# Performance work log

Hardware: AMD Instinct MI355X
Metric: run time of the kernel (lower is better)

Reference implementation:

```python
import jax, jax.numpy as jnp
import numpy as np

N = 100000
E = 1600000
F_IN, F_HID, F_OUT = 128, 32, 2


def setup_inputs() -> dict:
    key = jax.random.key(0)
    k1, k2, k3, k4 = jax.random.split(key, 4)
    x = jax.random.normal(k1, (N, F_IN), dtype=jnp.float32)
    edge_index = jax.random.randint(k2, (2, E), 0, N, dtype=jnp.int64)
    # Glorot-style init like torch_geometric GCNConv
    W1 = jax.random.normal(k3, (F_IN, F_HID), dtype=jnp.float32) * (1.0 / np.sqrt(F_IN))
    b1 = jnp.zeros((F_HID,), dtype=jnp.float32)
    W2 = jax.random.normal(k4, (F_HID, F_OUT), dtype=jnp.float32) * (1.0 / np.sqrt(F_HID))
    b2 = jnp.zeros((F_OUT,), dtype=jnp.float32)
    return {"x": x, "edge_index": edge_index, "W1": W1, "b1": b1, "W2": W2, "b2": b2}


def _gcn_conv(x, row, col, norm, W, b):
    # GCNConv: transform, then normalized aggregate (source -> target), then bias
    h = x @ W                                   # [N, F_out]
    msg = norm[:, None] * h[row]                # gather + scale, [E+N, F_out]
    out = jax.ops.segment_sum(msg, col, num_segments=N)  # scatter-add to targets
    return out + b


def reference(x, edge_index, W1, b1, W2, b2):
    # add self-loops (GCNConv default)
    loops = jnp.arange(N, dtype=edge_index.dtype)
    row = jnp.concatenate([edge_index[0], loops])
    col = jnp.concatenate([edge_index[1], loops])
    # symmetric normalization: deg^{-1/2}[row] * deg^{-1/2}[col], deg = in-degree w/ self-loops
    deg = jax.ops.segment_sum(jnp.ones_like(col, dtype=x.dtype), col, num_segments=N)
    dinv = jnp.where(deg > 0, jax.lax.rsqrt(deg), 0.0)
    norm = dinv[row] * dinv[col]                # [E+N]

    h = _gcn_conv(x, row, col, norm, W1, b1)
    h = jax.nn.relu(h)
    h = _gcn_conv(h, row, col, norm, W2, b2)
    return jax.nn.log_softmax(h, axis=1)
```

## Files before the change

kernel.cpp:

```cpp
#include <hip/hip_runtime.h>
#include <hip/hip_bf16.h>
#include <math.h>
#include <stdint.h>


#define GNN_N 100000
#define GNN_E 1600000
#define NBUCK 391
#define CAP 4608
#define CH 3125

typedef float fx2 __attribute__((ext_vector_type(2)));

__global__ __launch_bounds__(256) void k_bucket(const int* __restrict__ row,
                                                const int* __restrict__ col,
                                                int* __restrict__ bucket_fill,
                                                uint32_t* __restrict__ slab) {
    __shared__ int hist[NBUCK];
    __shared__ int base[NBUCK];
    const int tid = threadIdx.x;
    const int e0 = blockIdx.x * CH;

    int cc[13], rr[13];
    #pragma unroll
    for (int t = 0; t < 12; ++t) {
        cc[t] = col[e0 + tid + t * 256];
        rr[t] = row[e0 + tid + t * 256];
    }
    const bool has12 = (tid < CH - 12 * 256);
    if (has12) { cc[12] = col[e0 + tid + 3072]; rr[12] = row[e0 + tid + 3072]; }

    for (int i = tid; i < NBUCK; i += 256) hist[i] = 0;
    __syncthreads();
    #pragma unroll
    for (int t = 0; t < 12; ++t) atomicAdd(&hist[cc[t] >> 8], 1);
    if (has12) atomicAdd(&hist[cc[12] >> 8], 1);
    __syncthreads();
    for (int i = tid; i < NBUCK; i += 256) {
        int bb = (i + blockIdx.x * 131) % NBUCK;
        base[bb] = atomicAdd(&bucket_fill[bb], hist[bb]);
    }
    __syncthreads();
    #pragma unroll
    for (int t = 0; t < 12; ++t) {
        int b = cc[t] >> 8;
        int p = atomicAdd(&base[b], 1);
        if (p < CAP)
            slab[(size_t)b * CAP + p] = ((uint32_t)rr[t] << 8) | (uint32_t)(cc[t] & 255);
    }
    if (has12) {
        int b = cc[12] >> 8;
        int p = atomicAdd(&base[b], 1);
        if (p < CAP)
            slab[(size_t)b * CAP + p] = ((uint32_t)rr[12] << 8) | (uint32_t)(cc[12] & 255);
    }
}

__global__ __launch_bounds__(512) void k_fine(const uint32_t* __restrict__ slab,
                                              const int* __restrict__ bucket_fill,
                                              int* __restrict__ sorted_row,
                                              int* __restrict__ cnt,
                                              int* __restrict__ offsets,
                                              float* __restrict__ dinv, int n) {
    __shared__ int hist[256];
    __shared__ int excl[256];
    __shared__ int cur[256];
    __shared__ int wsum[4];
    __shared__ int s_gbase;
    __shared__ uint32_t stage[CAP];
    const int tid = threadIdx.x;
    const int b0 = blockIdx.x * 2;
    const int lane = tid & 63, wave = tid >> 6;

    if (tid < 64) {
        int s = 0;
        for (int i = tid; i < b0; i += 64) s += bucket_fill[i];
        #pragma unroll
        for (int m = 32; m >= 1; m >>= 1) s += __shfl_xor(s, m);
        if (tid == 0) s_gbase = s;
    }
    __syncthreads();
    int gbase = s_gbase;

    for (int pass = 0; pass < 2; ++pass) {
        const int b = b0 + pass;
        if (b >= NBUCK) break;
        const int nb = min(bucket_fill[b], CAP);
        const uint32_t* sl = slab + (size_t)b * CAP;

        if (tid < 256) { hist[tid] = 0; cur[tid] = 0; }
        __syncthreads();
        for (int i = tid; i < nb; i += 512)
            atomicAdd(&hist[sl[i] & 255u], 1);
        __syncthreads();
        int v = 0, inc = 0;
        if (tid < 256) {
            v = hist[tid];
            inc = v;
            #pragma unroll
            for (int d = 1; d < 64; d <<= 1) {
                int t = __shfl_up(inc, d);
                if (lane >= d) inc += t;
            }
            if (lane == 63) wsum[wave] = inc;
        }
        __syncthreads();
        if (tid == 0) {
            int a = 0;
            #pragma unroll
            for (int w = 0; w < 4; ++w) { int t = wsum[w]; wsum[w] = a; a += t; }
        }
        __syncthreads();
        if (tid < 256) {
            int ex = inc - v + wsum[wave];
            excl[tid] = ex;
            int c = b * 256 + tid;
            if (c < n) {
                cnt[c] = v;
                offsets[c] = gbase + ex;
                dinv[c] = rsqrtf((float)(v + 1));
            }
        }
        __syncthreads();
        for (int i = tid; i < nb; i += 512) {
            uint32_t u = sl[i];
            int f = (int)(u & 255u);
            int p = atomicAdd(&cur[f], 1);
            stage[excl[f] + p] = u >> 8;
        }
        __syncthreads();
        for (int i = tid; i < nb; i += 512)
            sorted_row[gbase + i] = (int)stage[i];
        gbase += nb;
        __syncthreads();
    }
}

#define MM1_NODES 64
__global__ __launch_bounds__(256) void k_matmul1(const float* __restrict__ x,
                                                 const float* __restrict__ W1,
                                                 const float* __restrict__ dinv,
                                                 uint32_t* __restrict__ h1q, int n) {
    __shared__ float xs[MM1_NODES * 129];
    __shared__ float w1s[128 * 32];
    const int tid = threadIdx.x;
    const int nodeBase = blockIdx.x * MM1_NODES;

    {
        const float4* w4 = (const float4*)W1;
        float4* s4 = (float4*)w1s;
        for (int i = tid; i < 1024; i += 256) s4[i] = w4[i];
    }
    {
        const float4* x4 = (const float4*)x;
        for (int i = tid; i < MM1_NODES * 32; i += 256) {
            int node = i >> 5;
            int k4 = i & 31;
            float4 v = make_float4(0.f, 0.f, 0.f, 0.f);
            if (nodeBase + node < n)
                v = x4[(size_t)(nodeBase + node) * 32 + k4];
            int bb = node * 129 + k4 * 4;
            xs[bb + 0] = v.x; xs[bb + 1] = v.y; xs[bb + 2] = v.z; xs[bb + 3] = v.w;
        }
    }
    __syncthreads();

    const int fg = tid & 7;
    const int ng = tid >> 3;
    const int n0 = ng * 2;
    float4 acc0 = make_float4(0.f, 0.f, 0.f, 0.f);
    float4 acc1 = make_float4(0.f, 0.f, 0.f, 0.f);
    const float4* w1s4 = (const float4*)w1s;
    const float* xr0 = &xs[n0 * 129];
    const float* xr1 = &xs[(n0 + 1) * 129];
    #pragma unroll 8
    for (int k = 0; k < 128; ++k) {
        float4 w = w1s4[k * 8 + fg];
        float a = xr0[k];
        float b = xr1[k];
        acc0.x += a * w.x; acc0.y += a * w.y; acc0.z += a * w.z; acc0.w += a * w.w;
        acc1.x += b * w.x; acc1.y += b * w.y; acc1.z += b * w.z; acc1.w += b * w.w;
    }
    int gn0 = nodeBase + n0;
    if (gn0 < n) {
        float d = dinv[gn0];
        int w = 0;
        w = __builtin_amdgcn_cvt_pk_fp8_f32(acc0.x * d, acc0.y * d, w, false);
        w = __builtin_amdgcn_cvt_pk_fp8_f32(acc0.z * d, acc0.w * d, w, true);
        h1q[(size_t)gn0 * 8 + fg] = (uint32_t)w;
    }
    if (gn0 + 1 < n) {
        float d = dinv[gn0 + 1];
        int w = 0;
        w = __builtin_amdgcn_cvt_pk_fp8_f32(acc1.x * d, acc1.y * d, w, false);
        w = __builtin_amdgcn_cvt_pk_fp8_f32(acc1.z * d, acc1.w * d, w, true);
        h1q[(size_t)(gn0 + 1) * 8 + fg] = (uint32_t)w;
    }
}

__device__ inline void fp8x16_acc(float* a, uint4 u) {
    fx2 p;
    p = __builtin_amdgcn_cvt_pk_f32_fp8(u.x, false); a[0] += p.x;  a[1] += p.y;
    p = __builtin_amdgcn_cvt_pk_f32_fp8(u.x, true);  a[2] += p.x;  a[3] += p.y;
    p = __builtin_amdgcn_cvt_pk_f32_fp8(u.y, false); a[4] += p.x;  a[5] += p.y;
    p = __builtin_amdgcn_cvt_pk_f32_fp8(u.y, true);  a[6] += p.x;  a[7] += p.y;
    p = __builtin_amdgcn_cvt_pk_f32_fp8(u.z, false); a[8] += p.x;  a[9] += p.y;
    p = __builtin_amdgcn_cvt_pk_f32_fp8(u.z, true);  a[10] += p.x; a[11] += p.y;
    p = __builtin_amdgcn_cvt_pk_f32_fp8(u.w, false); a[12] += p.x; a[13] += p.y;
    p = __builtin_amdgcn_cvt_pk_f32_fp8(u.w, true);  a[14] += p.x; a[15] += p.y;
}

__global__ __launch_bounds__(256) void k_gather1(const int* __restrict__ offsets,
                                                 const int* __restrict__ cnt,
                                                 const int* __restrict__ sorted_row,
                                                 const uint32_t* __restrict__ h1q,
                                                 const float* __restrict__ dinv,
                                                 const float* __restrict__ b1,
                                                 const float* __restrict__ W2,
                                                 float* __restrict__ h2s, int n) {
    __shared__ float sb1[32];
    __shared__ float sW2[64];
    const int tid = threadIdx.x;
    if (tid < 32) sb1[tid] = b1[tid];
    else if (tid < 96) sW2[tid - 32] = W2[tid - 32];
    __syncthreads();

    const int l = tid & 1;
    const int node = blockIdx.x * 128 + (tid >> 1);
    if (node >= n) return;
    const uint4* h4 = (const uint4*)h1q;
    float acc[16], acc2[16];
    #pragma unroll
    for (int j = 0; j < 16; ++j) { acc[j] = 0.f; acc2[j] = 0.f; }
    fp8x16_acc(acc, h4[(size_t)node * 2 + l]);
    const int start = offsets[node];
    const int deg = cnt[node];
    const int* sr = sorted_row + start;
    int k = 0;
    for (; k + 8 <= deg; k += 8) {
        int r[8];
        uint4 u[8];
        #pragma unroll
        for (int t = 0; t < 8; ++t) r[t] = sr[k + t];
        #pragma unroll
        for (int t = 0; t < 8; ++t) u[t] = h4[(size_t)r[t] * 2 + l];
        #pragma unroll
        for (int t = 0; t < 8; ++t) fp8x16_acc((t & 1) ? acc2 : acc, u[t]);
    }
    for (; k + 2 <= deg; k += 2) {
        int ra = sr[k], rb = sr[k + 1];
        uint4 ua = h4[(size_t)ra * 2 + l];
        uint4 ub = h4[(size_t)rb * 2 + l];
        fp8x16_acc(acc, ua);
        fp8x16_acc(acc2, ub);
    }
    if (k < deg)
        fp8x16_acc(acc, h4[(size_t)sr[k] * 2 + l]);
    #pragma unroll
    for (int j = 0; j < 16; ++j) acc[j] += acc2[j];

    const float dc = dinv[node];
    const int f0 = l * 16;
    float s0 = 0.f, s1 = 0.f;
    #pragma unroll
    for (int j = 0; j < 16; ++j) {
        float a = fmaxf(dc * acc[j] + sb1[f0 + j], 0.f);
        s0 += a * sW2[(f0 + j) * 2];
        s1 += a * sW2[(f0 + j) * 2 + 1];
    }
    s0 += __shfl_xor(s0, 1);
    s1 += __shfl_xor(s1, 1);
    if (l == 0) ((float2*)h2s)[node] = make_float2(dc * s0, dc * s1);
}

__global__ __launch_bounds__(256) void k_gather2(const int* __restrict__ offsets,
                                                 const int* __restrict__ cnt,
                                                 const int* __restrict__ sorted_row,
                                                 const float* __restrict__ h2s,
                                                 const float* __restrict__ dinv,
                                                 const float* __restrict__ b2,
                                                 float* __restrict__ out, int n) {
    const int tid = threadIdx.x;
    const int l = tid & 3;
    const int node = blockIdx.x * 64 + (tid >> 2);
    if (node >= n) return;
    const float2* h2 = (const float2*)h2s;
    float sx = 0.f, sy = 0.f;
    if (l == 0) { float2 s = h2[node]; sx = s.x; sy = s.y; }
    const int start = offsets[node];
    const int deg = cnt[node];
    for (int k = l; k < deg; k += 4) {
        float2 v = h2[sorted_row[start + k]];
        sx += v.x; sy += v.y;
    }
    sx += __shfl_xor(sx, 1); sx += __shfl_xor(sx, 2);
    sy += __shfl_xor(sy, 1); sy += __shfl_xor(sy, 2);
    if (l == 0) {
        float d = dinv[node];
        float v0 = d * sx + b2[0];
        float v1 = d * sy + b2[1];
        float m = fmaxf(v0, v1);
        float lg = m + logf(expf(v0 - m) + expf(v1 - m));
        ((float2*)out)[node] = make_float2(v0 - lg, v1 - lg);
    }
}

extern "C" void kernel_launch(void* const* d_in, const int* in_sizes, int n_in,
                              void* d_out, int out_size, void* d_ws, size_t ws_size,
                              hipStream_t stream) {
    const float* x  = (const float*)d_in[0];
    const int*   ei = (const int*)d_in[1];
    const float* W1 = (const float*)d_in[2];
    const float* b1 = (const float*)d_in[3];
    const float* W2 = (const float*)d_in[4];
    const float* b2 = (const float*)d_in[5];
    float* out = (float*)d_out;
    char* ws = (char*)d_ws;

    const int N = GNN_N;
    const int* row = ei;
    const int* col = ei + GNN_E;

    float*    dinv        = (float*)    ws;
    int*      cnt         = (int*)     (ws + 4ull *  100000);
    int*      offsets     = (int*)     (ws + 4ull *  200000);
    int*      bucket_fill = (int*)     (ws + 4ull *  300000);
    int*      sorted_row  = (int*)     (ws + 4ull *  300512);
    float*    h2s         = (float*)   (ws + 4ull * 1900512);
    uint32_t* h1q         = (uint32_t*)(ws + 4ull * 2100512);
    uint32_t* slab        = (uint32_t*)(ws + 4ull * 2900512);

    hipMemsetAsync(bucket_fill, 0, NBUCK * sizeof(int), stream);

    k_bucket <<<512, 256, 0, stream>>>(row, col, bucket_fill, slab);
    k_fine   <<<(NBUCK + 1) / 2, 512, 0, stream>>>(slab, bucket_fill, sorted_row, cnt, offsets, dinv, N);
    k_matmul1<<<(N + MM1_NODES - 1) / MM1_NODES, 256, 0, stream>>>(x, W1, dinv, h1q, N);
    k_gather1<<<(N + 127) / 128, 256, 0, stream>>>(offsets, cnt, sorted_row, h1q, dinv, b1, W2, h2s, N);
    k_gather2<<<(N + 63) / 64, 256, 0, stream>>>(offsets, cnt, sorted_row, h2s, dinv, b2, out, N);
}
```

Measured before the change: 179.8 us.

## Fuse fine bucket sort with first-layer matmul and derive degree from offsets

The fine counting-sort kernel and the first-layer dense transform are merged into one kernel with one block per 256-node bucket. Shared memory is reused between the sort staging area and the x/W1 tiles, and dinv comes from shared memory instead of global. The separate cnt array is removed: offsets gains a sentinel entry and the gather kernels compute degree as the difference of adjacent offsets. This saves a kernel launch and some global traffic, but the matmul now runs on only 391 blocks, which serialises four 64-node tiles per block and may lower parallelism.

```diff
diff --git a/kernel.cpp b/kernel.cpp
--- a/kernel.cpp
+++ b/kernel.cpp
@@ -56,145 +56,130 @@
     }
 }
 
-__global__ __launch_bounds__(512) void k_fine(const uint32_t* __restrict__ slab,
-                                              const int* __restrict__ bucket_fill,
-                                              int* __restrict__ sorted_row,
-                                              int* __restrict__ cnt,
-                                              int* __restrict__ offsets,
-                                              float* __restrict__ dinv, int n) {
-    __shared__ int hist[256];
-    __shared__ int excl[256];
-    __shared__ int cur[256];
+#define SMEM_BYTES 49408
+__global__ __launch_bounds__(512) void k_fine_mm(const uint32_t* __restrict__ slab,
+                                                 const int* __restrict__ bucket_fill,
+                                                 const float* __restrict__ x,
+                                                 const float* __restrict__ W1,
+                                                 int* __restrict__ sorted_row,
+                                                 int* __restrict__ offsets,
+                                                 float* __restrict__ dinv,
+                                                 uint32_t* __restrict__ h1q, int n) {
+    __shared__ alignas(16) char smem[SMEM_BYTES];
+    __shared__ float sdinv[256];
     __shared__ int wsum[4];
     __shared__ int s_gbase;
-    __shared__ uint32_t stage[CAP];
     const int tid = threadIdx.x;
-    const int b0 = blockIdx.x * 2;
+    const int b = blockIdx.x;
     const int lane = tid & 63, wave = tid >> 6;
 
+    int* hist = (int*)smem;
+    int* excl = hist + 256;
+    int* cur  = excl + 256;
+    uint32_t* stage = (uint32_t*)(cur + 256);
+
+    const int nb = min(bucket_fill[b], CAP);
+    const uint32_t* sl = slab + (size_t)b * CAP;
+
+    if (tid < 256) { hist[tid] = 0; cur[tid] = 0; }
     if (tid < 64) {
         int s = 0;
-        for (int i = tid; i < b0; i += 64) s += bucket_fill[i];
+        for (int i = tid; i < b; i += 64) s += bucket_fill[i];
         #pragma unroll
         for (int m = 32; m >= 1; m >>= 1) s += __shfl_xor(s, m);
         if (tid == 0) s_gbase = s;
     }
     __syncthreads();
-    int gbase = s_gbase;
-
-    for (int pass = 0; pass < 2; ++pass) {
-        const int b = b0 + pass;
-        if (b >= NBUCK) break;
-        const int nb = min(bucket_fill[b], CAP);
-        const uint32_t* sl = slab + (size_t)b * CAP;
-
-        if (tid < 256) { hist[tid] = 0; cur[tid] = 0; }
-        __syncthreads();
-        for (int i = tid; i < nb; i += 512)
-            atomicAdd(&hist[sl[i] & 255u], 1);
-        __syncthreads();
-        int v = 0, inc = 0;
-        if (tid < 256) {
-            v = hist[tid];
-            inc = v;
-            #pragma unroll
-            for (int d = 1; d < 64; d <<= 1) {
-                int t = __shfl_up(inc, d);
-                if (lane >= d) inc += t;
-            }
-            if (lane == 63) wsum[wave] = inc;
-        }
-        __syncthreads();
-        if (tid == 0) {
-            int a = 0;
-            #pragma unroll
-            for (int w = 0; w < 4; ++w) { int t = wsum[w]; wsum[w] = a; a += t; }
-        }
-        __syncthreads();
-        if (tid < 256) {
-            int ex = inc - v + wsum[wave];
-            excl[tid] = ex;
-            int c = b * 256 + tid;
-            if (c < n) {
-                cnt[c] = v;
-                offsets[c] = gbase + ex;
-                dinv[c] = rsqrtf((float)(v + 1));
-            }
-        }
-        __syncthreads();
-        for (int i = tid; i < nb; i += 512) {
-            uint32_t u = sl[i];
-            int f = (int)(u & 255u);
-            int p = atomicAdd(&cur[f], 1);
-            stage[excl[f] + p] = u >> 8;
-        }
-        __syncthreads();
-        for (int i = tid; i < nb; i += 512)
-            sorted_row[gbase + i] = (int)stage[i];
-        gbase += nb;
-        __syncthreads();
-    }
-}
-
-#define MM1_NODES 64
-__global__ __launch_bounds__(256) void k_matmul1(const float* __restrict__ x,
-                                                 const float* __restrict__ W1,
-                                                 const float* __restrict__ dinv,
-                                                 uint32_t* __restrict__ h1q, int n) {
-    __shared__ float xs[MM1_NODES * 129];
-    __shared__ float w1s[128 * 32];
-    const int tid = threadIdx.x;
-    const int nodeBase = blockIdx.x * MM1_NODES;
+    for (int i = tid; i < nb; i += 512)
+        atomicAdd(&hist[sl[i] & 255u], 1);
+    __syncthreads();
+    int v = 0, inc = 0;
+    if (tid < 256) {
+        v = hist[tid];
+        inc = v;
+        #pragma unroll
+        for (int d = 1; d < 64; d <<= 1) {
+            int t = __shfl_up(inc, d);
+            if (lane >= d) inc += t;
+        }
+        if (lane == 63) wsum[wave] = inc;
+    }
+    __syncthreads();
+    if (tid == 0) {
+        int a = 0;
+        #pragma unroll
+        for (int w = 0; w < 4; ++w) { int t = wsum[w]; wsum[w] = a; a += t; }
+    }
+    __syncthreads();
+    const int gbase = s_gbase;
+    if (tid < 256) {
+        int ex = inc - v + wsum[wave];
+        excl[tid] = ex;
+        float dv = rsqrtf((float)(v + 1));
+        sdinv[tid] = dv;
+        int c = b * 256 + tid;
+        if (c < n) {
+            offsets[c] = gbase + ex;
+            dinv[c] = dv;
+        }
+    }
+    if (b == NBUCK - 1 && tid == 256) offsets[n] = GNN_E;
+    __syncthreads();
+    for (int i = tid; i < nb; i += 512) {
+        uint32_t u = sl[i];
+        int f = (int)(u & 255u);
+        int p = atomicAdd(&cur[f], 1);
+        stage[excl[f] + p] = u >> 8;
+    }
+    __syncthreads();
+    for (int i = tid; i < nb; i += 512)
+        sorted_row[gbase + i] = (int)stage[i];
+    __syncthreads();
+
+    float* xs  = (float*)smem;
+    float* w1s = xs + 64 * 129;
 
     {
         const float4* w4 = (const float4*)W1;
         float4* s4 = (float4*)w1s;
-        for (int i = tid; i < 1024; i += 256) s4[i] = w4[i];
-    }
-    {
-        const float4* x4 = (const float4*)x;
-        for (int i = tid; i < MM1_NODES * 32; i += 256) {
-            int node = i >> 5;
-            int k4 = i & 31;
-            float4 v = make_float4(0.f, 0.f, 0.f, 0.f);
-            if (nodeBase + node < n)
-                v = x4[(size_t)(nodeBase + node) * 32 + k4];
-            int bb = node * 129 + k4 * 4;
-            xs[bb + 0] = v.x; xs[bb + 1] = v.y; xs[bb + 2] = v.z; xs[bb + 3] = v.w;
-        }
-    }
-    __syncthreads();
-
+        s4[tid] = w4[tid];
+        s4[tid + 512] = w4[tid + 512];
+    }
     const int fg = tid & 7;
-    const int ng = tid >> 3;
-    const int n0 = ng * 2;
-    float4 acc0 = make_float4(0.f, 0.f, 0.f, 0.f);
-    float4 acc1 = make_float4(0.f, 0.f, 0.f, 0.f);
-    const float4* w1s4 = (const float4*)w1s;
-    const float* xr0 = &xs[n0 * 129];
-    const float* xr1 = &xs[(n0 + 1) * 129];
-    #pragma unroll 8
-    for (int k = 0; k < 128; ++k) {
-        float4 w = w1s4[k * 8 + fg];
-        float a = xr0[k];
-        float b = xr1[k];
-        acc0.x += a * w.x; acc0.y += a * w.y; acc0.z += a * w.z; acc0.w += a * w.w;
-        acc1.x += b * w.x; acc1.y += b * w.y; acc1.z += b * w.z; acc1.w += b * w.w;
-    }
-    int gn0 = nodeBase + n0;
-    if (gn0 < n) {
-        float d = dinv[gn0];
-        int w = 0;
-        w = __builtin_amdgcn_cvt_pk_fp8_f32(acc0.x * d, acc0.y * d, w, false);
-        w = __builtin_amdgcn_cvt_pk_fp8_f32(acc0.z * d, acc0.w * d, w, true);
-        h1q[(size_t)gn0 * 8 + fg] = (uint32_t)w;
-    }
-    if (gn0 + 1 < n) {
-        float d = dinv[gn0 + 1];
-        int w = 0;
-        w = __builtin_amdgcn_cvt_pk_fp8_f32(acc1.x * d, acc1.y * d, w, false);
-        w = __builtin_amdgcn_cvt_pk_fp8_f32(acc1.z * d, acc1.w * d, w, true);
-        h1q[(size_t)(gn0 + 1) * 8 + fg] = (uint32_t)w;
+    const int nl = tid >> 3;
+    for (int s = 0; s < 4; ++s) {
+        const int tileBase = b * 256 + s * 64;
+        __syncthreads();
+        {
+            const float4* x4 = (const float4*)x;
+            for (int i = tid; i < 64 * 32; i += 512) {
+                int node = i >> 5;
+                int k4 = i & 31;
+                float4 vv = make_float4(0.f, 0.f, 0.f, 0.f);
+                if (tileBase + node < n)
+                    vv = x4[(size_t)(tileBase + node) * 32 + k4];
+                int bb = node * 129 + k4 * 4;
+                xs[bb + 0] = vv.x; xs[bb + 1] = vv.y; xs[bb + 2] = vv.z; xs[bb + 3] = vv.w;
+            }
+        }
+        __syncthreads();
+        float4 acc = make_float4(0.f, 0.f, 0.f, 0.f);
+        const float4* w1s4 = (const float4*)w1s;
+        const float* xr = &xs[nl * 129];
+        #pragma unroll 8
+        for (int k = 0; k < 128; ++k) {
+            float4 w = w1s4[k * 8 + fg];
+            float a = xr[k];
+            acc.x += a * w.x; acc.y += a * w.y; acc.z += a * w.z; acc.w += a * w.w;
+        }
+        int gn = tileBase + nl;
+        if (gn < n) {
+            float d = sdinv[s * 64 + nl];
+            int w = 0;
+            w = __builtin_amdgcn_cvt_pk_fp8_f32(acc.x * d, acc.y * d, w, false);
+            w = __builtin_amdgcn_cvt_pk_fp8_f32(acc.z * d, acc.w * d, w, true);
+            h1q[(size_t)gn * 8 + fg] = (uint32_t)w;
+        }
     }
 }
 
@@ -211,7 +196,6 @@
 }
 
 __global__ __launch_bounds__(256) void k_gather1(const int* __restrict__ offsets,
-                                                 const int* __restrict__ cnt,
                                                  const int* __restrict__ sorted_row,
                                                  const uint32_t* __restrict__ h1q,
                                                  const float* __restrict__ dinv,
@@ -234,7 +218,7 @@
     for (int j = 0; j < 16; ++j) { acc[j] = 0.f; acc2[j] = 0.f; }
     fp8x16_acc(acc, h4[(size_t)node * 2 + l]);
     const int start = offsets[node];
-    const int deg = cnt[node];
+    const int deg = offsets[node + 1] - start;
     const int* sr = sorted_row + start;
     int k = 0;
     for (; k + 8 <= deg; k += 8) {
@@ -274,7 +258,6 @@
 }
 
 __global__ __launch_bounds__(256) void k_gather2(const int* __restrict__ offsets,
-                                                 const int* __restrict__ cnt,
                                                  const int* __restrict__ sorted_row,
                                                  const float* __restrict__ h2s,
                                                  const float* __restrict__ dinv,
@@ -288,7 +271,7 @@
     float sx = 0.f, sy = 0.f;
     if (l == 0) { float2 s = h2[node]; sx = s.x; sy = s.y; }
     const int start = offsets[node];
-    const int deg = cnt[node];
+    const int deg = offsets[node + 1] - start;
     for (int k = l; k < deg; k += 4) {
         float2 v = h2[sorted_row[start + k]];
         sx += v.x; sy += v.y;
@@ -322,19 +305,18 @@
     const int* col = ei + GNN_E;
 
     float*    dinv        = (float*)    ws;
-    int*      cnt         = (int*)     (ws + 4ull *  100000);
-    int*      offsets     = (int*)     (ws + 4ull *  200000);
-    int*      bucket_fill = (int*)     (ws + 4ull *  300000);
-    int*      sorted_row  = (int*)     (ws + 4ull *  300512);
-    float*    h2s         = (float*)   (ws + 4ull * 1900512);
-    uint32_t* h1q         = (uint32_t*)(ws + 4ull * 2100512);
-    uint32_t* slab        = (uint32_t*)(ws + 4ull * 2900512);
+    int*      offsets     = (int*)     (ws + 4ull *  100000);
+    int*      bucket_fill = (int*)     (ws + 4ull *  200512);
+    int*      sorted_row  = (int*)     (ws + 4ull *  201024);
+    float*    h2s         = (float*)   (ws + 4ull * 1801024);
+    uint32_t* h1q         = (uint32_t*)(ws + 4ull * 2001024);
+    uint32_t* slab        = (uint32_t*)(ws + 4ull * 2801024);
 
     hipMemsetAsync(bucket_fill, 0, NBUCK * sizeof(int), stream);
 
     k_bucket <<<512, 256, 0, stream>>>(row, col, bucket_fill, slab);
-    k_fine   <<<(NBUCK + 1) / 2, 512, 0, stream>>>(slab, bucket_fill, sorted_row, cnt, offsets, dinv, N);
-    k_matmul1<<<(N + MM1_NODES - 1) / MM1_NODES, 256, 0, stream>>>(x, W1, dinv, h1q, N);
-    k_gather1<<<(N + 127) / 128, 256, 0, stream>>>(offsets, cnt, sorted_row, h1q, dinv, b1, W2, h2s, N);
-    k_gather2<<<(N + 63) / 64, 256, 0, stream>>>(offsets, cnt, sorted_row, h2s, dinv, b2, out, N);
-}
+    k_fine_mm<<<NBUCK, 512, 0, stream>>>(slab, bucket_fill, x, W1,
+                                         sorted_row, offsets, dinv, h1q, N);
+    k_gather1<<<(N + 127) / 128, 256, 0, stream>>>(offsets, sorted_row, h1q, dinv, b1, W2, h2s, N);
+    k_gather2<<<(N + 63) / 64, 256, 0, stream>>>(offsets, sorted_row, h2s, dinv, b2, out, N);
+}
```

Measured after the change: 182.3 us. Within noise of the previous version (+1.4%).

## Vectorize bucket loads, reuse histogram ranks, drop cnt array for offset differences

Applied to the files above, without the earlier changes.

The bucketing kernel now loads col/row with int4 vector loads over 4096-edge chunks and keeps the rank returned by the shared histogram atomic, so the scatter pass skips its second LDS atomic. The fine sort does the same: it caches slab entries in registers along with their histogram ranks, so it neither reloads them nor uses a second atomic counter array. The cnt array is removed; degrees come from offsets[node+1]-offsets[node], with a sentinel written at offsets[n]. This saves global traffic and atomics in the CSR build, at the cost of more registers and a tail-block path.

```diff
diff --git a/kernel.cpp b/kernel.cpp
--- a/kernel.cpp
+++ b/kernel.cpp
@@ -8,69 +8,95 @@
 #define GNN_E 1600000
 #define NBUCK 391
 #define CAP 4608
-#define CH 3125
+#define CHB 4096
 
 typedef float fx2 __attribute__((ext_vector_type(2)));
 
 __global__ __launch_bounds__(256) void k_bucket(const int* __restrict__ row,
                                                 const int* __restrict__ col,
                                                 int* __restrict__ bucket_fill,
-                                                uint32_t* __restrict__ slab) {
+                                                uint32_t* __restrict__ slab, int e) {
     __shared__ int hist[NBUCK];
     __shared__ int base[NBUCK];
     const int tid = threadIdx.x;
-    const int e0 = blockIdx.x * CH;
-
-    int cc[13], rr[13];
-    #pragma unroll
-    for (int t = 0; t < 12; ++t) {
-        cc[t] = col[e0 + tid + t * 256];
-        rr[t] = row[e0 + tid + t * 256];
-    }
-    const bool has12 = (tid < CH - 12 * 256);
-    if (has12) { cc[12] = col[e0 + tid + 3072]; rr[12] = row[e0 + tid + 3072]; }
+    const int e0 = blockIdx.x * CHB;
+    const int m = min(CHB, e - e0);
+    const bool full = (m == CHB);
 
     for (int i = tid; i < NBUCK; i += 256) hist[i] = 0;
-    __syncthreads();
-    #pragma unroll
-    for (int t = 0; t < 12; ++t) atomicAdd(&hist[cc[t] >> 8], 1);
-    if (has12) atomicAdd(&hist[cc[12] >> 8], 1);
+
+    int cc[16], rr[16], pp[16];
+    if (full) {
+        const int4* c4 = (const int4*)(col + e0);
+        const int4* r4 = (const int4*)(row + e0);
+        #pragma unroll
+        for (int t = 0; t < 4; ++t) {
+            int4 c = c4[tid + t * 256];
+            int4 r = r4[tid + t * 256];
+            cc[t * 4 + 0] = c.x; cc[t * 4 + 1] = c.y;
+            cc[t * 4 + 2] = c.z; cc[t * 4 + 3] = c.w;
+            rr[t * 4 + 0] = r.x; rr[t * 4 + 1] = r.y;
+            rr[t * 4 + 2] = r.z; rr[t * 4 + 3] = r.w;
+        }
+        __syncthreads();
+        #pragma unroll
+        for (int t = 0; t < 16; ++t)
+            pp[t] = atomicAdd(&hist[cc[t] >> 8], 1);
+    } else {
+        __syncthreads();
+        #pragma unroll
+        for (int t = 0; t < 16; ++t) {
+            int i = tid + t * 256;
+            if (i < m) {
+                cc[t] = col[e0 + i];
+                rr[t] = row[e0 + i];
+                pp[t] = atomicAdd(&hist[cc[t] >> 8], 1);
+            }
+        }
+    }
     __syncthreads();
     for (int i = tid; i < NBUCK; i += 256) {
         int bb = (i + blockIdx.x * 131) % NBUCK;
         base[bb] = atomicAdd(&bucket_fill[bb], hist[bb]);
     }
     __syncthreads();
-    #pragma unroll
-    for (int t = 0; t < 12; ++t) {
-        int b = cc[t] >> 8;
-        int p = atomicAdd(&base[b], 1);
-        if (p < CAP)
-            slab[(size_t)b * CAP + p] = ((uint32_t)rr[t] << 8) | (uint32_t)(cc[t] & 255);
-    }
-    if (has12) {
-        int b = cc[12] >> 8;
-        int p = atomicAdd(&base[b], 1);
-        if (p < CAP)
-            slab[(size_t)b * CAP + p] = ((uint32_t)rr[12] << 8) | (uint32_t)(cc[12] & 255);
+    if (full) {
+        #pragma unroll
+        for (int t = 0; t < 16; ++t) {
+            int b = cc[t] >> 8;
+            int p = base[b] + pp[t];
+            if (p < CAP)
+                slab[(size_t)b * CAP + p] = ((uint32_t)rr[t] << 8) | (uint32_t)(cc[t] & 255);
+        }
+    } else {
+        #pragma unroll
+        for (int t = 0; t < 16; ++t) {
+            int i = tid + t * 256;
+            if (i < m) {
+                int b = cc[t] >> 8;
+                int p = base[b] + pp[t];
+                if (p < CAP)
+                    slab[(size_t)b * CAP + p] = ((uint32_t)rr[t] << 8) | (uint32_t)(cc[t] & 255);
+            }
+        }
     }
 }
 
 __global__ __launch_bounds__(512) void k_fine(const uint32_t* __restrict__ slab,
                                               const int* __restrict__ bucket_fill,
                                               int* __restrict__ sorted_row,
-                                              int* __restrict__ cnt,
                                               int* __restrict__ offsets,
                                               float* __restrict__ dinv, int n) {
     __shared__ int hist[256];
     __shared__ int excl[256];
-    __shared__ int cur[256];
     __shared__ int wsum[4];
     __shared__ int s_gbase;
     __shared__ uint32_t stage[CAP];
     const int tid = threadIdx.x;
     const int b0 = blockIdx.x * 2;
     const int lane = tid & 63, wave = tid >> 6;
+
+    if (blockIdx.x == gridDim.x - 1 && tid == 511) offsets[n] = GNN_E;
 
     if (tid < 64) {
         int s = 0;
@@ -88,10 +114,19 @@
         const int nb = min(bucket_fill[b], CAP);
         const uint32_t* sl = slab + (size_t)b * CAP;
 
-        if (tid < 256) { hist[tid] = 0; cur[tid] = 0; }
-        __syncthreads();
-        for (int i = tid; i < nb; i += 512)
-            atomicAdd(&hist[sl[i] & 255u], 1);
+        if (tid < 256) hist[tid] = 0;
+        __syncthreads();
+        uint32_t uu[9];
+        int pp[9];
+        #pragma unroll
+        for (int j = 0; j < 9; ++j) {
+            int i = tid + j * 512;
+            if (i < nb) {
+                uint32_t u = sl[i];
+                uu[j] = u;
+                pp[j] = atomicAdd(&hist[u & 255u], 1);
+            }
+        }
         __syncthreads();
         int v = 0, inc = 0;
         if (tid < 256) {
@@ -116,17 +151,16 @@
             excl[tid] = ex;
             int c = b * 256 + tid;
             if (c < n) {
-                cnt[c] = v;
                 offsets[c] = gbase + ex;
                 dinv[c] = rsqrtf((float)(v + 1));
             }
         }
         __syncthreads();
-        for (int i = tid; i < nb; i += 512) {
-            uint32_t u = sl[i];
-            int f = (int)(u & 255u);
-            int p = atomicAdd(&cur[f], 1);
-            stage[excl[f] + p] = u >> 8;
+        #pragma unroll
+        for (int j = 0; j < 9; ++j) {
+            int i = tid + j * 512;
+            if (i < nb)
+                stage[excl[uu[j] & 255u] + pp[j]] = uu[j] >> 8;
         }
         __syncthreads();
         for (int i = tid; i < nb; i += 512)
@@ -211,7 +245,6 @@
 }
 
 __global__ __launch_bounds__(256) void k_gather1(const int* __restrict__ offsets,
-                                                 const int* __restrict__ cnt,
                                                  const int* __restrict__ sorted_row,
                                                  const uint32_t* __restrict__ h1q,
                                                  const float* __restrict__ dinv,
@@ -234,7 +267,7 @@
     for (int j = 0; j < 16; ++j) { acc[j] = 0.f; acc2[j] = 0.f; }
     fp8x16_acc(acc, h4[(size_t)node * 2 + l]);
     const int start = offsets[node];
-    const int deg = cnt[node];
+    const int deg = offsets[node + 1] - start;
     const int* sr = sorted_row + start;
     int k = 0;
     for (; k + 8 <= deg; k += 8) {
@@ -274,7 +307,6 @@
 }
 
 __global__ __launch_bounds__(256) void k_gather2(const int* __restrict__ offsets,
-                                                 const int* __restrict__ cnt,
                                                  const int* __restrict__ sorted_row,
                                                  const float* __restrict__ h2s,
                                                  const float* __restrict__ dinv,
@@ -288,7 +320,7 @@
     float sx = 0.f, sy = 0.f;
     if (l == 0) { float2 s = h2[node]; sx = s.x; sy = s.y; }
     const int start = offsets[node];
-    const int deg = cnt[node];
+    const int deg = offsets[node + 1] - start;
     for (int k = l; k < deg; k += 4) {
         float2 v = h2[sorted_row[start + k]];
         sx += v.x; sy += v.y;
@@ -310,31 +342,30 @@
                               hipStream_t stream) {
     const float* x  = (const float*)d_in[0];
     const int*   ei = (const int*)d_in[1];
+    const float* b1 = (const float*)d_in[3];
     const float* W1 = (const float*)d_in[2];
-    const float* b1 = (const float*)d_in[3];
     const float* W2 = (const float*)d_in[4];
     const float* b2 = (const float*)d_in[5];
     float* out = (float*)d_out;
     char* ws = (char*)d_ws;
 
-    const int N = GNN_N;
+    const int N = GNN_N, E = GNN_E;
     const int* row = ei;
     const int* col = ei + GNN_E;
 
     float*    dinv        = (float*)    ws;
-    int*      cnt         = (int*)     (ws + 4ull *  100000);
-    int*      offsets     = (int*)     (ws + 4ull *  200000);
-    int*      bucket_fill = (int*)     (ws + 4ull *  300000);
-    int*      sorted_row  = (int*)     (ws + 4ull *  300512);
-    float*    h2s         = (float*)   (ws + 4ull * 1900512);
-    uint32_t* h1q         = (uint32_t*)(ws + 4ull * 2100512);
-    uint32_t* slab        = (uint32_t*)(ws + 4ull * 2900512);
+    int*      offsets     = (int*)     (ws + 4ull *  100000);
+    int*      bucket_fill = (int*)     (ws + 4ull *  200512);
+    int*      sorted_row  = (int*)     (ws + 4ull *  201024);
+    float*    h2s         = (float*)   (ws + 4ull * 1801024);
+    uint32_t* h1q         = (uint32_t*)(ws + 4ull * 2001024);
+    uint32_t* slab        = (uint32_t*)(ws + 4ull * 2801024);
 
     hipMemsetAsync(bucket_fill, 0, NBUCK * sizeof(int), stream);
 
-    k_bucket <<<512, 256, 0, stream>>>(row, col, bucket_fill, slab);
-    k_fine   <<<(NBUCK + 1) / 2, 512, 0, stream>>>(slab, bucket_fill, sorted_row, cnt, offsets, dinv, N);
+    k_bucket <<<(E + CHB - 1) / CHB, 256, 0, stream>>>(row, col, bucket_fill, slab, E);
+    k_fine   <<<(NBUCK + 1) / 2, 512, 0, stream>>>(slab, bucket_fill, sorted_row, offsets, dinv, N);
     k_matmul1<<<(N + MM1_NODES - 1) / MM1_NODES, 256, 0, stream>>>(x, W1, dinv, h1q, N);
-    k_gather1<<<(N + 127) / 128, 256, 0, stream>>>(offsets, cnt, sorted_row, h1q, dinv, b1, W2, h2s, N);
-    k_gather2<<<(N + 63) / 64, 256, 0, stream>>>(offsets, cnt, sorted_row, h2s, dinv, b2, out, N);
-}
+    k_gather1<<<(N + 127) / 128, 256, 0, stream>>>(offsets, sorted_row, h1q, dinv, b1, W2, h2s, N);
+    k_gather2<<<(N + 63) / 64, 256, 0, stream>>>(offsets, sorted_row, h2s, dinv, b2, out, N);
+}
```

Result: no change. 178.3 us (-0.8%).
